# Kernel optimization log

Hardware: AMD Instinct MI355X
Metric: run time of the kernel (lower is better)

The kernel has to match this reference:

```python
import jax, jax.numpy as jnp
import numpy as np

B, T, C, H = 2, 2048, 1024, 16
HD = C // H  # head dim = 64


def setup_inputs() -> dict:
    key = jax.random.key(0)
    ks = jax.random.split(key, 9)
    s = 1.0 / np.sqrt(C)
    return {
        "x": jax.random.normal(ks[0], (B, T, C), dtype=jnp.float32),
        "Wq": jax.random.normal(ks[1], (C, C), dtype=jnp.float32) * s,
        "bq": jax.random.normal(ks[2], (C,), dtype=jnp.float32) * 0.02,
        "Wk": jax.random.normal(ks[3], (C, C), dtype=jnp.float32) * s,
        "bk": jax.random.normal(ks[4], (C,), dtype=jnp.float32) * 0.02,
        "Wv": jax.random.normal(ks[5], (C, C), dtype=jnp.float32) * s,
        "bv": jax.random.normal(ks[6], (C,), dtype=jnp.float32) * 0.02,
        "Wo": jax.random.normal(ks[7], (C, C), dtype=jnp.float32) * s,
        "bo": jax.random.normal(ks[8], (C,), dtype=jnp.float32) * 0.02,
    }


def reference(x, Wq, bq, Wk, bk, Wv, bv, Wo, bo):
    # Projections (torch Linear: x @ W.T + b; here W stored pre-transposed as [C_in, C_out])
    q = x @ Wq + bq  # (B,T,C)
    k = x @ Wk + bk
    v = x @ Wv + bv
    # Split heads: (B,T,C) -> (B,H,T,HD)
    q = q.reshape(B, T, H, HD).transpose(0, 2, 1, 3)
    k = k.reshape(B, T, H, HD).transpose(0, 2, 1, 3)
    v = v.reshape(B, T, H, HD).transpose(0, 2, 1, 3)
    # NOTE: original module never applies a causal mask despite its name.
    score = jnp.einsum("bhqd,bhkd->bhqk", q, k) / jnp.sqrt(jnp.float32(HD))
    score = jax.nn.softmax(score, axis=-1)
    y = jnp.einsum("bhqk,bhkd->bhqd", score, v)
    y = y.transpose(0, 2, 1, 3).reshape(B, T, C)
    # dropout is identity in eval mode
    return y @ Wo + bo
```

## Files before the change

kernel.cpp:

```cpp
#include <hip/hip_runtime.h>
#include <math.h>

#define B_ 2
#define T_ 2048
#define C_ 1024
#define H_ 16
#define HD_ 64
#define M_ (B_*T_)

typedef _Float16 half2v __attribute__((ext_vector_type(2)));
typedef _Float16 half4v __attribute__((ext_vector_type(4)));
typedef _Float16 half8v __attribute__((ext_vector_type(8)));
typedef float f32x4 __attribute__((ext_vector_type(4)));

#define GLD_LDS(gp, lp) \
  __builtin_amdgcn_global_load_lds( \
      (const __attribute__((address_space(1))) void*)(gp), \
      (__attribute__((address_space(3))) void*)(lp), 16, 0, 0)

__global__ __launch_bounds__(256) void prep_kernel(
    const float* __restrict__ x,
    const float* __restrict__ Wq, const float* __restrict__ Wk,
    const float* __restrict__ Wv, const float* __restrict__ Wo,
    const float* __restrict__ bq, const float* __restrict__ bk,
    const float* __restrict__ bv,
    _Float16* __restrict__ xh, _Float16* __restrict__ Wt3,
    _Float16* __restrict__ Wot, float* __restrict__ b3)
{
  __shared__ float tile[32][33];
  const int blk = blockIdx.x, thr = threadIdx.x;
  if (blk < 4096) {
    int i = blk * 256 + thr;
    float4 v = ((const float4*)x)[i];
    half4v h; h[0] = (_Float16)v.x; h[1] = (_Float16)v.y;
    h[2] = (_Float16)v.z; h[3] = (_Float16)v.w;
    ((half4v*)xh)[i] = h;
  } else if (blk < 8192) {
    int zz = (blk - 4096) >> 10;
    int bxy = (blk - 4096) & 1023;
    const float* W; _Float16* Wt;
    switch (zz) {
      case 0:  W = Wq; Wt = Wt3; break;
      case 1:  W = Wk; Wt = Wt3 + (size_t)1024 * 1024; break;
      case 2:  W = Wv; Wt = Wt3 + (size_t)2048 * 1024; break;
      default: W = Wo; Wt = Wot; break;
    }
    const int n0 = (bxy & 31) * 32, k0 = (bxy >> 5) * 32;
    const int tx = thr & 31, ty = thr >> 5;
#pragma unroll
    for (int r = 0; r < 4; r++) {
      int k = ty + r * 8;
      tile[k][tx] = W[(size_t)(k0 + k) * C_ + n0 + tx];
    }
    __syncthreads();
#pragma unroll
    for (int r = 0; r < 4; r++) {
      int n = ty + r * 8;
      Wt[(size_t)(n0 + n) * C_ + k0 + tx] = (_Float16)tile[tx][n];
    }
  } else {
    int i = (blk - 8192) * 256 + thr;
    const float* s = (i < 1024) ? bq : ((i < 2048) ? bk : bv);
    b3[i] = s[i & 1023];
  }
}

template <int BM, int BN, int EPI>
__global__ __launch_bounds__(256) void gemm_f16_kernel(
    const _Float16* __restrict__ A, const _Float16* __restrict__ Bw,
    const float* __restrict__ bias,
    _Float16* __restrict__ o0, _Float16* __restrict__ o1,
    _Float16* __restrict__ o2, float* __restrict__ of)
{
  constexpr int FM = BM / 32, FN = BN / 32;
  __shared__ __align__(16) _Float16 As[BM * 32];
  __shared__ __align__(16) _Float16 Bs[BN * 32];
  const int t = threadIdx.x;
  const int w = t >> 6, lane = t & 63, l15 = lane & 15, quad = lane >> 4;
  const int wm = (w & 1) * (BM / 2), wn = (w >> 1) * (BN / 2);
  const int bm = blockIdx.y * BM, bn = blockIdx.x * BN;
  const int lrow = lane >> 2, lcol = (lane & 3) * 8;

  f32x4 acc[FM][FN];
#pragma unroll
  for (int i = 0; i < FM; i++)
#pragma unroll
    for (int j = 0; j < FN; j++) acc[i][j] = (f32x4){0.f, 0.f, 0.f, 0.f};

  for (int k0 = 0; k0 < 1024; k0 += 32) {
#pragma unroll
    for (int i = 0; i < BM / 64; i++) {
      int ca = w + 4 * i;
      int row = ca * 16 + lrow;
      GLD_LDS(A + (size_t)(bm + row) * 1024 + k0 + lcol, As + ca * 512);
    }
#pragma unroll
    for (int i = 0; i < BN / 64; i++) {
      int cb = w + 4 * i;
      int row = cb * 16 + lrow;
      GLD_LDS(Bw + (size_t)(bn + row) * 1024 + k0 + lcol, Bs + cb * 512);
    }
    __syncthreads();

    half8v af[FM], bf[FN];
#pragma unroll
    for (int mt = 0; mt < FM; mt++)
      af[mt] = *(const half8v*)(As + (wm + mt * 16 + l15) * 32 + quad * 8);
#pragma unroll
    for (int nt = 0; nt < FN; nt++)
      bf[nt] = *(const half8v*)(Bs + (wn + nt * 16 + l15) * 32 + quad * 8);
#pragma unroll
    for (int mt = 0; mt < FM; mt++)
#pragma unroll
      for (int nt = 0; nt < FN; nt++)
        acc[mt][nt] = __builtin_amdgcn_mfma_f32_16x16x32_f16(
            af[mt], bf[nt], acc[mt][nt], 0, 0, 0);
    __syncthreads();
  }

#pragma unroll
  for (int mt = 0; mt < FM; mt++)
#pragma unroll
    for (int nt = 0; nt < FN; nt++) {
      int n = bn + wn + nt * 16 + l15;
      float bv = bias[n];
      if (EPI == 0 && bn >= 2048) {
        int dg = n - 2048;
        int hh = dg >> 6, hd = dg & 63;
        int m0 = bm + wm + mt * 16 + quad * 4;
        int bb = m0 >> 11, tt = m0 & 2047;
        half2v p01 = __builtin_bit_cast(half2v,
            __builtin_amdgcn_cvt_pkrtz(acc[mt][nt][0] + bv, acc[mt][nt][1] + bv));
        half2v p23 = __builtin_bit_cast(half2v,
            __builtin_amdgcn_cvt_pkrtz(acc[mt][nt][2] + bv, acc[mt][nt][3] + bv));
        half4v pk = __builtin_shufflevector(p01, p23, 0, 1, 2, 3);
        *(half4v*)(o2 + (((size_t)(bb * H_ + hh) * 64 + hd) * 2048 + tt)) = pk;
      } else {
#pragma unroll
        for (int r = 0; r < 4; r++) {
          int m = bm + wm + mt * 16 + quad * 4 + r;
          float v = acc[mt][nt][r] + bv;
          if (EPI == 0) {
            if (bn < 1024) {
              o0[(size_t)m * 1024 + n] = (_Float16)(v * 0.180336884f);
            } else {
              o1[(size_t)m * 1024 + (n - 1024)] = (_Float16)v;
            }
          } else {
            of[(size_t)m * 1024 + n] = v;
          }
        }
      }
    }
}

__global__ __launch_bounds__(256) void attn_f16_kernel(
    const _Float16* __restrict__ Qh, const _Float16* __restrict__ Kh,
    const _Float16* __restrict__ Vt, _Float16* __restrict__ part0,
    _Float16* __restrict__ part1, float* __restrict__ ml)
{
  __shared__ __align__(16) _Float16 Ks[64 * 68];
  __shared__ __align__(16) _Float16 Vs[64 * 68];
  const int t = threadIdx.x;
  const int w = t >> 6, lane = t & 63, l15 = lane & 15, quad = lane >> 4;
  const int qt = blockIdx.x, h = blockIdx.y;
  const int b = blockIdx.z >> 1, half = blockIdx.z & 1;
  const int qg = qt * 64 + w * 16 + l15;
  const size_t qoff = ((size_t)(b * T_ + qg)) * C_ + h * HD_;

  half8v qf[2];
  qf[0] = *(const half8v*)(Qh + qoff + quad * 8);
  qf[1] = *(const half8v*)(Qh + qoff + 32 + quad * 8);

  f32x4 o[4];
#pragma unroll
  for (int i = 0; i < 4; i++) o[i] = (f32x4){0.f, 0.f, 0.f, 0.f};
  float m_run = -INFINITY, l_run = 0.f;

  const size_t kbase = ((size_t)b * T_) * C_ + h * HD_;
  const size_t vbase = ((size_t)(b * H_ + h)) * HD_ * 2048;

  const int srow = t >> 3, scp = t & 7;
  const int k0g = half * 1024;

  for (int kt0 = 0; kt0 < 1024; kt0 += 64) {
    const int kg = k0g + kt0;
#pragma unroll
    for (int i = 0; i < 2; i++) {
      int row = srow + i * 32;
      *(uint4*)((char*)Ks + row * 136 + scp * 16) =
          *(const uint4*)(Kh + kbase + (size_t)(kg + row) * C_ + scp * 8);
      *(uint4*)((char*)Vs + row * 136 + scp * 16) =
          *(const uint4*)(Vt + vbase + (size_t)row * 2048 + kg + scp * 8);
    }
    __syncthreads();

    f32x4 s[4];
#pragma unroll
    for (int kt = 0; kt < 4; kt++) {
      s[kt] = (f32x4){0.f, 0.f, 0.f, 0.f};
      int key = kt * 16 + l15;
#pragma unroll
      for (int ks = 0; ks < 2; ks++) {
        half8v kf = *(const half8v*)((char*)Ks + key * 136 + (ks * 4 + quad) * 16);
        s[kt] = __builtin_amdgcn_mfma_f32_16x16x32_f16(kf, qf[ks], s[kt], 0, 0, 0);
      }
    }

    float tmax = -INFINITY;
#pragma unroll
    for (int kt = 0; kt < 4; kt++)
#pragma unroll
      for (int r = 0; r < 4; r++) tmax = fmaxf(tmax, s[kt][r]);
    tmax = fmaxf(tmax, __shfl_xor(tmax, 16));
    tmax = fmaxf(tmax, __shfl_xor(tmax, 32));
    float mnew = fmaxf(m_run, tmax);
    float alpha = __builtin_amdgcn_exp2f(m_run - mnew);

    float psum = 0.f;
    half4v pf[4];
#pragma unroll
    for (int kt = 0; kt < 4; kt++) {
      float p0 = __builtin_amdgcn_exp2f(s[kt][0] - mnew);
      float p1 = __builtin_amdgcn_exp2f(s[kt][1] - mnew);
      float p2 = __builtin_amdgcn_exp2f(s[kt][2] - mnew);
      float p3 = __builtin_amdgcn_exp2f(s[kt][3] - mnew);
      psum += (p0 + p1) + (p2 + p3);
      half2v pk01 = __builtin_bit_cast(half2v, __builtin_amdgcn_cvt_pkrtz(p0, p1));
      half2v pk23 = __builtin_bit_cast(half2v, __builtin_amdgcn_cvt_pkrtz(p2, p3));
      pf[kt] = __builtin_shufflevector(pk01, pk23, 0, 1, 2, 3);
    }
    psum += __shfl_xor(psum, 16);
    psum += __shfl_xor(psum, 32);
    l_run = l_run * alpha + psum;
    m_run = mnew;
#pragma unroll
    for (int dt = 0; dt < 4; dt++) o[dt] *= alpha;

#pragma unroll
    for (int dt = 0; dt < 4; dt++) {
      int d = dt * 16 + l15;
#pragma unroll
      for (int kt = 0; kt < 4; kt++) {
        half4v vf = *(const half4v*)((char*)Vs + d * 136 + kt * 32 + quad * 8);
        o[dt] = __builtin_amdgcn_mfma_f32_16x16x16f16(vf, pf[kt], o[dt], 0, 0, 0);
      }
    }
    __syncthreads();
  }

  float inv = 1.0f / l_run;
  _Float16* pp = half ? part1 : part0;
  const int q = w * 16 + l15;
  const size_t pbase = ((((size_t)(b * H_ + h)) * 32 + qt) * 64 + q) * 64;
#pragma unroll
  for (int dt = 0; dt < 4; dt++) {
    half4v yv;
#pragma unroll
    for (int r = 0; r < 4; r++) yv[r] = (_Float16)(o[dt][r] * inv);
    *(half4v*)(pp + pbase + dt * 16 + quad * 4) = yv;
  }
  if (quad == 0) {
    size_t mlb = (size_t)half * 131072 +
                 ((((size_t)(b * H_ + h)) * 32 + qt) * 64 + q) * 2;
    ml[mlb] = m_run; ml[mlb + 1] = l_run;
  }
}

__global__ __launch_bounds__(256) void attn_merge_kernel(
    const _Float16* __restrict__ part0, const _Float16* __restrict__ part1,
    const float* __restrict__ ml, _Float16* __restrict__ Yh)
{
  const int qt = blockIdx.x, h = blockIdx.y, b = blockIdx.z;
  const int t = threadIdx.x;
  const int q = t >> 2, dc = (t & 3) * 16;
  const size_t rowi = (((size_t)(b * H_ + h)) * 32 + qt) * 64 + q;
  const size_t pbase = rowi * 64 + dc;
  float m0 = ml[rowi * 2], l0 = ml[rowi * 2 + 1];
  float m1 = ml[131072 + rowi * 2], l1 = ml[131072 + rowi * 2 + 1];
  float m = fmaxf(m0, m1);
  float a0 = __builtin_amdgcn_exp2f(m0 - m) * l0;
  float a1 = __builtin_amdgcn_exp2f(m1 - m) * l1;
  float inv = 1.0f / (a0 + a1);
  float w0 = a0 * inv, w1 = a1 * inv;
  half8v x0a = *(const half8v*)(part0 + pbase);
  half8v x0b = *(const half8v*)(part0 + pbase + 8);
  half8v x1a = *(const half8v*)(part1 + pbase);
  half8v x1b = *(const half8v*)(part1 + pbase + 8);
  half8v ya, yb;
#pragma unroll
  for (int j = 0; j < 8; j++) {
    ya[j] = (_Float16)(w0 * (float)x0a[j] + w1 * (float)x1a[j]);
    yb[j] = (_Float16)(w0 * (float)x0b[j] + w1 * (float)x1b[j]);
  }
  _Float16* yp = Yh + ((size_t)(b * T_ + qt * 64 + q)) * C_ + h * HD_ + dc;
  *(half8v*)yp = ya;
  *(half8v*)(yp + 8) = yb;
}

extern "C" void kernel_launch(void* const* d_in, const int* in_sizes, int n_in,
                              void* d_out, int out_size, void* d_ws, size_t ws_size,
                              hipStream_t stream) {
  const float* x  = (const float*)d_in[0];
  const float* Wq = (const float*)d_in[1];
  const float* bq = (const float*)d_in[2];
  const float* Wk = (const float*)d_in[3];
  const float* bk = (const float*)d_in[4];
  const float* Wv = (const float*)d_in[5];
  const float* bv = (const float*)d_in[6];
  const float* Wo = (const float*)d_in[7];
  const float* bo = (const float*)d_in[8];
  float* out = (float*)d_out;

  char* ws = (char*)d_ws;
  _Float16* xh    = (_Float16*)(ws);
  _Float16* Qh    = (_Float16*)(ws + (((size_t)8)  << 20));
  _Float16* Kh    = (_Float16*)(ws + (((size_t)16) << 20));
  _Float16* Vt    = (_Float16*)(ws + (((size_t)24) << 20));
  _Float16* part0 = (_Float16*)(ws + (((size_t)32) << 20));
  _Float16* part1 = xh;
  _Float16* Ym    = Kh;
  _Float16* Wt3   = (_Float16*)(ws + (((size_t)40) << 20));
  _Float16* Wot   = (_Float16*)(ws + (((size_t)46) << 20));
  float*    b3    = (float*)   (ws + (((size_t)48) << 20));
  float*    ml    = (float*)   (ws + (((size_t)48) << 20) + 65536);

  prep_kernel<<<8204, 256, 0, stream>>>(x, Wq, Wk, Wv, Wo, bq, bk, bv,
                                        xh, Wt3, Wot, b3);

  gemm_f16_kernel<128, 128, 0><<<dim3(24, 32), 256, 0, stream>>>(
      xh, Wt3, b3, Qh, Kh, Vt, nullptr);

  attn_f16_kernel<<<dim3(32, 16, 4), 256, 0, stream>>>(
      Qh, Kh, Vt, part0, part1, ml);
  attn_merge_kernel<<<dim3(32, 16, 2), 256, 0, stream>>>(part0, part1, ml, Ym);

  gemm_f16_kernel<64, 128, 1><<<dim3(8, 64), 256, 0, stream>>>(
      Ym, Wot, bo, nullptr, nullptr, nullptr, out);
}
```

Measured before the change: 234.9 us.

## Process two query tiles per wave in attention to reuse K/V fragments

The attention kernel now runs 2 waves (128 threads) per block instead of 4, and each wave handles two 16-row query groups. Each K and V fragment read from LDS feeds two MFMAs, halving LDS traffic per unit of compute and giving more independent MFMAs per wave. The cost is roughly double the accumulator and score registers per wave, which may reduce occupancy, and fewer waves per block to hide latency; each thread also does twice the global-to-LDS staging.

```diff
diff --git a/kernel.cpp b/kernel.cpp
--- a/kernel.cpp
+++ b/kernel.cpp
@@ -154,7 +154,7 @@
     }
 }
 
-__global__ __launch_bounds__(256) void attn_f16_kernel(
+__global__ __launch_bounds__(128) void attn_f16_kernel(
     const _Float16* __restrict__ Qh, const _Float16* __restrict__ Kh,
     const _Float16* __restrict__ Vt, _Float16* __restrict__ part0,
     _Float16* __restrict__ part1, float* __restrict__ ml)
@@ -162,80 +162,92 @@
   __shared__ __align__(16) _Float16 Ks[64 * 68];
   __shared__ __align__(16) _Float16 Vs[64 * 68];
   const int t = threadIdx.x;
-  const int w = t >> 6, lane = t & 63, l15 = lane & 15, quad = lane >> 4;
+  const int w = t >> 6;
+  const int lane = t & 63, l15 = lane & 15, quad = lane >> 4;
   const int qt = blockIdx.x, h = blockIdx.y;
   const int b = blockIdx.z >> 1, half = blockIdx.z & 1;
-  const int qg = qt * 64 + w * 16 + l15;
-  const size_t qoff = ((size_t)(b * T_ + qg)) * C_ + h * HD_;
-
-  half8v qf[2];
-  qf[0] = *(const half8v*)(Qh + qoff + quad * 8);
-  qf[1] = *(const half8v*)(Qh + qoff + 32 + quad * 8);
-
-  f32x4 o[4];
-#pragma unroll
-  for (int i = 0; i < 4; i++) o[i] = (f32x4){0.f, 0.f, 0.f, 0.f};
-  float m_run = -INFINITY, l_run = 0.f;
+
+  size_t qoff[2];
+  half8v qf[2][2];
+#pragma unroll
+  for (int g = 0; g < 2; g++) {
+    int qg = qt * 64 + (w * 2 + g) * 16 + l15;
+    qoff[g] = ((size_t)(b * T_ + qg)) * C_ + h * HD_;
+    qf[g][0] = *(const half8v*)(Qh + qoff[g] + quad * 8);
+    qf[g][1] = *(const half8v*)(Qh + qoff[g] + 32 + quad * 8);
+  }
+
+  f32x4 o[2][4];
+#pragma unroll
+  for (int g = 0; g < 2; g++)
+#pragma unroll
+    for (int i = 0; i < 4; i++) o[g][i] = (f32x4){0.f, 0.f, 0.f, 0.f};
+  float m_run[2] = {-INFINITY, -INFINITY}, l_run[2] = {0.f, 0.f};
 
   const size_t kbase = ((size_t)b * T_) * C_ + h * HD_;
   const size_t vbase = ((size_t)(b * H_ + h)) * HD_ * 2048;
-
-  const int srow = t >> 3, scp = t & 7;
   const int k0g = half * 1024;
 
   for (int kt0 = 0; kt0 < 1024; kt0 += 64) {
     const int kg = k0g + kt0;
 #pragma unroll
-    for (int i = 0; i < 2; i++) {
-      int row = srow + i * 32;
-      *(uint4*)((char*)Ks + row * 136 + scp * 16) =
-          *(const uint4*)(Kh + kbase + (size_t)(kg + row) * C_ + scp * 8);
-      *(uint4*)((char*)Vs + row * 136 + scp * 16) =
-          *(const uint4*)(Vt + vbase + (size_t)row * 2048 + kg + scp * 8);
-    }
-    __syncthreads();
-
-    f32x4 s[4];
+    for (int i = 0; i < 4; i++) {
+      int slot = t + i * 128;
+      int row = slot >> 3, cp = slot & 7;
+      *(uint4*)((char*)Ks + row * 136 + cp * 16) =
+          *(const uint4*)(Kh + kbase + (size_t)(kg + row) * C_ + cp * 8);
+      *(uint4*)((char*)Vs + row * 136 + cp * 16) =
+          *(const uint4*)(Vt + vbase + (size_t)row * 2048 + kg + cp * 8);
+    }
+    __syncthreads();
+
+    f32x4 s0[4], s1[4];
 #pragma unroll
     for (int kt = 0; kt < 4; kt++) {
-      s[kt] = (f32x4){0.f, 0.f, 0.f, 0.f};
+      s0[kt] = (f32x4){0.f, 0.f, 0.f, 0.f};
+      s1[kt] = (f32x4){0.f, 0.f, 0.f, 0.f};
       int key = kt * 16 + l15;
 #pragma unroll
       for (int ks = 0; ks < 2; ks++) {
         half8v kf = *(const half8v*)((char*)Ks + key * 136 + (ks * 4 + quad) * 16);
-        s[kt] = __builtin_amdgcn_mfma_f32_16x16x32_f16(kf, qf[ks], s[kt], 0, 0, 0);
+        s0[kt] = __builtin_amdgcn_mfma_f32_16x16x32_f16(kf, qf[0][ks], s0[kt], 0, 0, 0);
+        s1[kt] = __builtin_amdgcn_mfma_f32_16x16x32_f16(kf, qf[1][ks], s1[kt], 0, 0, 0);
       }
     }
 
-    float tmax = -INFINITY;
-#pragma unroll
-    for (int kt = 0; kt < 4; kt++)
-#pragma unroll
-      for (int r = 0; r < 4; r++) tmax = fmaxf(tmax, s[kt][r]);
-    tmax = fmaxf(tmax, __shfl_xor(tmax, 16));
-    tmax = fmaxf(tmax, __shfl_xor(tmax, 32));
-    float mnew = fmaxf(m_run, tmax);
-    float alpha = __builtin_amdgcn_exp2f(m_run - mnew);
-
-    float psum = 0.f;
-    half4v pf[4];
-#pragma unroll
-    for (int kt = 0; kt < 4; kt++) {
-      float p0 = __builtin_amdgcn_exp2f(s[kt][0] - mnew);
-      float p1 = __builtin_amdgcn_exp2f(s[kt][1] - mnew);
-      float p2 = __builtin_amdgcn_exp2f(s[kt][2] - mnew);
-      float p3 = __builtin_amdgcn_exp2f(s[kt][3] - mnew);
-      psum += (p0 + p1) + (p2 + p3);
-      half2v pk01 = __builtin_bit_cast(half2v, __builtin_amdgcn_cvt_pkrtz(p0, p1));
-      half2v pk23 = __builtin_bit_cast(half2v, __builtin_amdgcn_cvt_pkrtz(p2, p3));
-      pf[kt] = __builtin_shufflevector(pk01, pk23, 0, 1, 2, 3);
-    }
-    psum += __shfl_xor(psum, 16);
-    psum += __shfl_xor(psum, 32);
-    l_run = l_run * alpha + psum;
-    m_run = mnew;
-#pragma unroll
-    for (int dt = 0; dt < 4; dt++) o[dt] *= alpha;
+    half4v pf[2][4];
+#pragma unroll
+    for (int g = 0; g < 2; g++) {
+      f32x4* s = g ? s1 : s0;
+      float tmax = -INFINITY;
+#pragma unroll
+      for (int kt = 0; kt < 4; kt++)
+#pragma unroll
+        for (int r = 0; r < 4; r++) tmax = fmaxf(tmax, s[kt][r]);
+      tmax = fmaxf(tmax, __shfl_xor(tmax, 16));
+      tmax = fmaxf(tmax, __shfl_xor(tmax, 32));
+      float mnew = fmaxf(m_run[g], tmax);
+      float alpha = __builtin_amdgcn_exp2f(m_run[g] - mnew);
+
+      float psum = 0.f;
+#pragma unroll
+      for (int kt = 0; kt < 4; kt++) {
+        float p0 = __builtin_amdgcn_exp2f(s[kt][0] - mnew);
+        float p1 = __builtin_amdgcn_exp2f(s[kt][1] - mnew);
+        float p2 = __builtin_amdgcn_exp2f(s[kt][2] - mnew);
+        float p3 = __builtin_amdgcn_exp2f(s[kt][3] - mnew);
+        psum += (p0 + p1) + (p2 + p3);
+        half2v pk01 = __builtin_bit_cast(half2v, __builtin_amdgcn_cvt_pkrtz(p0, p1));
+        half2v pk23 = __builtin_bit_cast(half2v, __builtin_amdgcn_cvt_pkrtz(p2, p3));
+        pf[g][kt] = __builtin_shufflevector(pk01, pk23, 0, 1, 2, 3);
+      }
+      psum += __shfl_xor(psum, 16);
+      psum += __shfl_xor(psum, 32);
+      l_run[g] = l_run[g] * alpha + psum;
+      m_run[g] = mnew;
+#pragma unroll
+      for (int dt = 0; dt < 4; dt++) o[g][dt] *= alpha;
+    }
 
 #pragma unroll
     for (int dt = 0; dt < 4; dt++) {
@@ -243,27 +255,31 @@
 #pragma unroll
       for (int kt = 0; kt < 4; kt++) {
         half4v vf = *(const half4v*)((char*)Vs + d * 136 + kt * 32 + quad * 8);
-        o[dt] = __builtin_amdgcn_mfma_f32_16x16x16f16(vf, pf[kt], o[dt], 0, 0, 0);
+        o[0][dt] = __builtin_amdgcn_mfma_f32_16x16x16f16(vf, pf[0][kt], o[0][dt], 0, 0, 0);
+        o[1][dt] = __builtin_amdgcn_mfma_f32_16x16x16f16(vf, pf[1][kt], o[1][dt], 0, 0, 0);
       }
     }
     __syncthreads();
   }
 
-  float inv = 1.0f / l_run;
   _Float16* pp = half ? part1 : part0;
-  const int q = w * 16 + l15;
-  const size_t pbase = ((((size_t)(b * H_ + h)) * 32 + qt) * 64 + q) * 64;
-#pragma unroll
-  for (int dt = 0; dt < 4; dt++) {
-    half4v yv;
-#pragma unroll
-    for (int r = 0; r < 4; r++) yv[r] = (_Float16)(o[dt][r] * inv);
-    *(half4v*)(pp + pbase + dt * 16 + quad * 4) = yv;
-  }
-  if (quad == 0) {
-    size_t mlb = (size_t)half * 131072 +
-                 ((((size_t)(b * H_ + h)) * 32 + qt) * 64 + q) * 2;
-    ml[mlb] = m_run; ml[mlb + 1] = l_run;
+#pragma unroll
+  for (int g = 0; g < 2; g++) {
+    float inv = 1.0f / l_run[g];
+    const int q = (w * 2 + g) * 16 + l15;
+    const size_t pbase = ((((size_t)(b * H_ + h)) * 32 + qt) * 64 + q) * 64;
+#pragma unroll
+    for (int dt = 0; dt < 4; dt++) {
+      half4v yv;
+#pragma unroll
+      for (int r = 0; r < 4; r++) yv[r] = (_Float16)(o[g][dt][r] * inv);
+      *(half4v*)(pp + pbase + dt * 16 + quad * 4) = yv;
+    }
+    if (quad == 0) {
+      size_t mlb = (size_t)half * 131072 +
+                   ((((size_t)(b * H_ + h)) * 32 + qt) * 64 + q) * 2;
+      ml[mlb] = m_run[g]; ml[mlb + 1] = l_run[g];
+    }
   }
 }
 
@@ -331,7 +347,7 @@
   gemm_f16_kernel<128, 128, 0><<<dim3(24, 32), 256, 0, stream>>>(
       xh, Wt3, b3, Qh, Kh, Vt, nullptr);
 
-  attn_f16_kernel<<<dim3(32, 16, 4), 256, 0, stream>>>(
+  attn_f16_kernel<<<dim3(32, 16, 4), 128, 0, stream>>>(
       Qh, Kh, Vt, part0, part1, ml);
   attn_merge_kernel<<<dim3(32, 16, 2), 256, 0, stream>>>(part0, part1, ml, Ym);
 
```

Result: slower. 278.5 us (+18.6%).
